# Performance work log

Measured on AMD Instinct MI355X. Metric: run time of the kernel, lower is better.

The kernel has to match this reference:

```python
import jax, jax.numpy as jnp
import numpy as np

H = 450    # hidden_size (JTNN default)
LAT = 56   # latent_size (tree_vec dim)
V = 780    # vocab size
T = 1024   # n_trees
L = 24     # nodes per tree (path topology)


def _tree_meta(Ln):
    # forward edge i: (i, i+1) eid=i ; reverse edge i: (i+1, i) eid=(Ln-1)+i
    n_f = Ln - 1
    eids, preds, srcs, dsts, labels = [], [], [], [], []
    for i in range(n_f):  # forward DFS steps
        eids.append(i); srcs.append(i); dsts.append(i + 1)
        preds.append(i - 1 if i > 0 else -1); labels.append(0)
    for k in range(n_f):  # backtrack DFS steps (reverse edges, deepest first)
        i = n_f - 1 - k
        eids.append(n_f + i); srcs.append(i + 1); dsts.append(i)
        preds.append(n_f + i + 1 if i < n_f - 1 else -1); labels.append(1)
    # incoming edges of the dst node v (for the node 'pull' h = sum of m)
    in1 = [d - 1 if d > 0 else -1 for d in dsts]
    in2 = [n_f + d if d < n_f else -1 for d in dsts]
    meta = [np.asarray(a, np.int32) for a in (eids, preds, srcs, dsts, in1, in2)]
    return meta, np.asarray(labels, np.float32)


def setup_inputs():
    key = jax.random.key(0)
    ks = jax.random.split(key, 12)
    s = 0.05
    return {
        "wid": jax.random.randint(ks[0], (T, L), 0, V, dtype=jnp.int32),
        "tree_vec": jax.random.normal(ks[1], (T, LAT), jnp.float32),
        "emb": jax.random.normal(ks[2], (V, H)) * s,
        "W_w": jax.random.normal(ks[3], (H + LAT, H)) * s, "W_b": jnp.zeros((H,)),
        "U_w": jax.random.normal(ks[4], (2 * H + LAT, H)) * s, "U_b": jnp.zeros((H,)),
        "Wo_w": jax.random.normal(ks[5], (H, V)) * s, "Wo_b": jnp.zeros((V,)),
        "Us_w": jax.random.normal(ks[6], (H, 1)) * s, "Us_b": jnp.zeros((1,)),
        "Wz_w": jax.random.normal(ks[7], (2 * H, H)) * s, "Wz_b": jnp.zeros((H,)),
        "Wr_w": jax.random.normal(ks[8], (H, H)) * s,
        "Ur_w": jax.random.normal(ks[9], (H, H)) * s, "Ur_b": jnp.zeros((H,)),
        "Wh_w": jax.random.normal(ks[10], (2 * H, H)) * s, "Wh_b": jnp.zeros((H,)),
    }


def reference(wid, tree_vec, emb, W_w, W_b, U_w, U_b, Wo_w, Wo_b, Us_w, Us_b,
              Wz_w, Wz_b, Wr_w, Ur_w, Ur_b, Wh_w, Wh_b):
    Tn, Ln = wid.shape
    n_f = Ln - 1
    nE = 2 * n_f
    meta, labels = _tree_meta(Ln)
    xs = tuple(jnp.asarray(a) for a in meta)
    x = emb[wid]                                  # [T, L, H] node features
    m0 = jnp.zeros((Tn, nE, H), x.dtype)
    rm0 = jnp.zeros((Tn, nE, H), x.dtype)

    def step(carry, sx_):
        m, rm = carry
        eid, pred, src, dst, i1, i2 = sx_
        gp = jnp.maximum(pred, 0)
        s = jnp.where(pred >= 0, m[:, gp], 0.0)        # line-graph pull: sum of m
        arm = jnp.where(pred >= 0, rm[:, gp], 0.0)     # accum_rm
        sxn = x[:, src]                                # src_x
        dxn = x[:, dst]                                # dst_x
        z = jax.nn.sigmoid(jnp.concatenate([sxn, s], 1) @ Wz_w + Wz_b)
        mt = jnp.tanh(jnp.concatenate([sxn, arm], 1) @ Wh_w + Wh_b)
        m_new = (1.0 - z) * s + z * mt
        r = jax.nn.sigmoid(dxn @ Wr_w + m_new @ Ur_w + Ur_b)
        m = m.at[:, eid].set(m_new)
        rm = rm.at[:, eid].set(r * m_new)
        # node pull on v: h_v = sum of m over incoming edges (post edge update)
        h_v = (jnp.where(i1 >= 0, m[:, jnp.maximum(i1, 0)], 0.0)
               + jnp.where(i2 >= 0, m[:, jnp.maximum(i2, 0)], 0.0))
        return (m, rm), (h_v, dxn)

    (_, _), (hs, xvs) = jax.lax.scan(step, (m0, rm0), xs)  # [nE, T, H] each

    tv_steps = jnp.broadcast_to(tree_vec, (nE, Tn, LAT))
    p_in = jnp.concatenate([
        jnp.concatenate([x[:, 0], jnp.zeros((Tn, H), x.dtype), tree_vec], 1),
        jnp.concatenate([xvs, hs, tv_steps], -1).reshape(-1, 2 * H + LAT),
    ], 0)
    q_in = jnp.concatenate([
        jnp.concatenate([jnp.zeros((Tn, H), x.dtype), tree_vec], 1),
        jnp.concatenate([hs[:n_f], tv_steps[:n_f]], -1).reshape(-1, H + LAT),
    ], 0)
    p_targets = jnp.concatenate([jnp.repeat(jnp.asarray(1.0 - labels), Tn),
                                 jnp.zeros((Tn,), jnp.float32)])
    q_targets = wid.T.reshape(-1)

    q_logits = jax.nn.relu(q_in @ W_w + W_b) @ Wo_w + Wo_b
    p_logit = (jax.nn.relu(p_in @ U_w + U_b) @ Us_w + Us_b)[:, 0]
    p_loss = jnp.sum(p_targets * jax.nn.softplus(-p_logit)
                     + (1.0 - p_targets) * jax.nn.softplus(p_logit)) / Tn
    logp = jax.nn.log_softmax(q_logits, -1)
    q_loss = -jnp.sum(jnp.take_along_axis(logp, q_targets[:, None], 1)) / Tn
    p_acc = jnp.mean(((p_logit > 0).astype(jnp.int32) == p_targets.astype(jnp.int32)).astype(jnp.float32))
    q_acc = jnp.mean((jnp.argmax(q_logits, 1) == q_targets).astype(jnp.float32))
    return (q_loss, p_loss, q_acc, p_acc)
```

## Files before the change

kernel.cpp:

```cpp
#include <hip/hip_runtime.h>
#include <hip/hip_bf16.h>
#include <math.h>

#define H 450
#define HP 464
#define KP 480
#define LAT 56
#define V 780
#define LW 24
#define NE 46
#define NF 23
#define SLOT (1024*HP)
#define SROWS 2048
#define QROWS (24*1024)
#define PROWS (47*1024)
#define PTGT  (23*1024)
#define QBLK 6144
#define XBSZ ((size_t)QROWS * HP)
#define BTROWS 5312

typedef __hip_bfloat16 bf16;
typedef __attribute__((ext_vector_type(8))) short short8;
typedef __attribute__((ext_vector_type(4))) float f32x4;

#define MFMA16(a,b,c) __builtin_amdgcn_mfma_f32_16x16x32_bf16(a,b,c,0,0,0)

__device__ __forceinline__ float sigm_f(float x) { return 1.f / (1.f + __expf(-x)); }
__device__ __forceinline__ float tanh_f(float x) { return 2.f / (1.f + __expf(-2.f * x)) - 1.f; }
__device__ __forceinline__ float toF(bf16 x) { return __bfloat162float(x); }
__device__ __forceinline__ void stV(float* p, float v) { *p = v; }
__device__ __forceinline__ void stV(bf16* p, float v) { *p = __float2bfloat16(v); }
__device__ __forceinline__ short8 ld8(const bf16* p) { return *reinterpret_cast<const short8*>(p); }

__device__ __forceinline__ void gl_lds(const bf16* g, bf16* l) {
    __builtin_amdgcn_global_load_lds(
        (const __attribute__((address_space(1))) void*)g,
        (__attribute__((address_space(3))) void*)l, 16, 0, 0);
}

__device__ __forceinline__ void xcd_decode128(int b, int C, int& row0, int& col0) {
    int rres = b & 7;
    int colt = (b >> 3) % C;
    int g    = b / (8 * C);
    row0 = (rres + 8 * g) * 128;
    col0 = colt * 128;
}

__global__ __launch_bounds__(256)
void prep_w(const float* __restrict__ Wz, const float* __restrict__ Wh,
            const float* __restrict__ Wr, const float* __restrict__ Uw,
            const float* __restrict__ Ww, const float* __restrict__ Wo,
            const float* __restrict__ Ur, bf16* __restrict__ BT) {
    int idx = blockIdx.x * 256 + threadIdx.x;
    if (idx >= BTROWS * KP) return;
    int r = idx / KP, k = idx - r * KP;
    const float* src; int n; int N = H; int ld = H;
    if (r < 1856) {
        if (r < 450)       { src = Wz; n = r; }
        else if (r < 900)  { src = Wh; n = r - 450; }
        else if (r < 1350) { src = Wr; n = r - 900; }
        else               { src = Uw; n = r - 1350; }
    } else if (r < 2368) { src = Wz + 450 * 450; n = r - 1856; }
    else if (r < 2880)   { src = Wh + 450 * 450; n = r - 2368; }
    else if (r < 3392)   { src = Ur;             n = r - 2880; }
    else if (r < 3904)   { src = Uw + 450 * 450; n = r - 3392; }
    else if (r < 4416)   { src = Ww;             n = r - 3904; }
    else                 { src = Wo; n = r - 4416; N = V; ld = V; }
    float v = (n < N && k < H) ? src[(size_t)k * ld + n] : 0.f;
    BT[idx] = __float2bfloat16(v);
}

__global__ __launch_bounds__(256)
void pack_misc(const float* __restrict__ zb, const float* __restrict__ hb,
               const float* __restrict__ rb, float* __restrict__ bias4,
               float* __restrict__ out) {
    int i = blockIdx.x * 256 + threadIdx.x;
    if (i < 4) out[i] = 0.f;
    if (i >= 1856) return;
    float v = 0.f;
    if (i < 450)       v = zb[i];
    else if (i < 900)  v = hb[i - 450];
    else if (i < 1350) v = rb[i - 900];
    bias4[i] = v;
}

__global__ __launch_bounds__(256)
void gather_x(const float* __restrict__ emb, const int* __restrict__ wid,
              bf16* __restrict__ x_all) {
    int e = blockIdx.x * 256 + threadIdx.x;
    if (e >= 24 * 1024 * 225) return;
    int row = e / 225, h2 = e - row * 225;
    int t = row >> 10, n = row & 1023;
    int v = wid[n * LW + t];
    float2 x = ((const float2*)(emb + (size_t)v * H))[h2];
    bf16* dst = x_all + (size_t)row * HP + 2 * h2;
    dst[0] = __float2bfloat16(x.x);
    dst[1] = __float2bfloat16(x.y);
}

template<typename TC>
__global__ __launch_bounds__(256)
void gemm128(const bf16* __restrict__ A, int lda,
             const bf16* __restrict__ Bt, int N, int cblk,
             TC* __restrict__ C, int ldc,
             const float* __restrict__ bias,
             const float* __restrict__ addrow, int addld, int relu) {
    __shared__ bf16 As[128 * 32];
    __shared__ bf16 Bs[128 * 32];
    int tid = threadIdx.x;
    int lane = tid & 63, wave = tid >> 6;
    int wx = wave & 1, wy = wave >> 1;
    int lrow = lane & 15, quad = lane >> 4;
    int perm = ((quad + (lrow >> 1)) & 3) * 8;
    int row0, col0;
    xcd_decode128(blockIdx.x, cblk, row0, col0);
    f32x4 acc[4][4] = {};
    for (int k0i = 0; k0i < 15; k0i++) {
        int k0 = k0i * 32;
#pragma unroll
        for (int r = 0; r < 2; r++) {
            int tt = r * 256 + tid;
            int row = tt >> 2, cl = tt & 3;
            int cg = (cl - (row >> 1)) & 3;
            gl_lds(A  + (size_t)(row0 + row) * lda + k0 + cg * 8, As + tt * 8);
            gl_lds(Bt + (size_t)(col0 + row) * KP  + k0 + cg * 8, Bs + tt * 8);
        }
        __syncthreads();
        short8 a[4], b[4];
#pragma unroll
        for (int f = 0; f < 4; f++)
            a[f] = ld8(As + (wy * 64 + f * 16 + lrow) * 32 + perm);
#pragma unroll
        for (int f = 0; f < 4; f++)
            b[f] = ld8(Bs + (wx * 64 + f * 16 + lrow) * 32 + perm);
#pragma unroll
        for (int fi = 0; fi < 4; fi++)
#pragma unroll
            for (int fj = 0; fj < 4; fj++)
                acc[fi][fj] = MFMA16(a[fi], b[fj], acc[fi][fj]);
        __syncthreads();
    }
#pragma unroll
    for (int fi = 0; fi < 4; fi++)
#pragma unroll
        for (int e = 0; e < 4; e++) {
            int r = row0 + wy * 64 + fi * 16 + quad * 4 + e;
#pragma unroll
            for (int fj = 0; fj < 4; fj++) {
                int c = col0 + wx * 64 + fj * 16 + lrow;
                if (c >= N) continue;
                float v = acc[fi][fj][e];
                if (bias) v += bias[c];
                if (addrow) v += addrow[(size_t)(r & 1023) * addld + c];
                if (relu) v = fmaxf(v, 0.f);
                stV(&C[(size_t)r * ldc + c], v);
            }
        }
}

__global__ __launch_bounds__(256)
void gemm128_pre(const bf16* __restrict__ A,
                 const bf16* __restrict__ Bt,
                 bf16* __restrict__ X0,
                 const float* __restrict__ bias4) {
    __shared__ bf16 As[128 * 32];
    __shared__ bf16 Bs[128 * 32];
    int tid = threadIdx.x;
    int lane = tid & 63, wave = tid >> 6;
    int wx = wave & 1, wy = wave >> 1;
    int lrow = lane & 15, quad = lane >> 4;
    int perm = ((quad + (lrow >> 1)) & 3) * 8;
    int row0, col0;
    xcd_decode128(blockIdx.x, 15, row0, col0);
    f32x4 acc[4][4] = {};
    for (int k0i = 0; k0i < 15; k0i++) {
        int k0 = k0i * 32;
#pragma unroll
        for (int r = 0; r < 2; r++) {
            int tt = r * 256 + tid;
            int row = tt >> 2, cl = tt & 3;
            int cg = (cl - (row >> 1)) & 3;
            gl_lds(A  + (size_t)(row0 + row) * HP + k0 + cg * 8, As + tt * 8);
            gl_lds(Bt + (size_t)(col0 + row) * KP + k0 + cg * 8, Bs + tt * 8);
        }
        __syncthreads();
        short8 a[4], b[4];
#pragma unroll
        for (int f = 0; f < 4; f++)
            a[f] = ld8(As + (wy * 64 + f * 16 + lrow) * 32 + perm);
#pragma unroll
        for (int f = 0; f < 4; f++)
            b[f] = ld8(Bs + (wx * 64 + f * 16 + lrow) * 32 + perm);
#pragma unroll
        for (int fi = 0; fi < 4; fi++)
#pragma unroll
            for (int fj = 0; fj < 4; fj++)
                acc[fi][fj] = MFMA16(a[fi], b[fj], acc[fi][fj]);
        __syncthreads();
    }
#pragma unroll
    for (int fi = 0; fi < 4; fi++)
#pragma unroll
        for (int e = 0; e < 4; e++) {
            int r = row0 + wy * 64 + fi * 16 + quad * 4 + e;
#pragma unroll
            for (int fj = 0; fj < 4; fj++) {
                int c = col0 + wx * 64 + fj * 16 + lrow;
                if (c >= 1800) continue;
                int mm = c / 450;
                int cc = c - mm * 450;
                float v = acc[fi][fj][e] + bias4[c];
                X0[(size_t)mm * XBSZ + (size_t)r * HP + cc] = __float2bfloat16(v);
            }
        }
}

__global__ __launch_bounds__(256)
void p_gemm128(const bf16* __restrict__ hs, const bf16* __restrict__ UbT,
               const bf16* __restrict__ XUa, const float* __restrict__ Ptv,
               const float* __restrict__ Us, float* __restrict__ pl) {
    __shared__ bf16 As[128 * 32];
    __shared__ bf16 Bs[128 * 32];
    int tid = threadIdx.x;
    int lane = tid & 63, wave = tid >> 6;
    int wx = wave & 1, wy = wave >> 1;
    int lrow = lane & 15, quad = lane >> 4;
    int perm = ((quad + (lrow >> 1)) & 3) * 8;
    int row0, col0;
    xcd_decode128(blockIdx.x, 4, row0, col0);
    f32x4 acc[4][4] = {};
    for (int k0i = 0; k0i < 15; k0i++) {
        int k0 = k0i * 32;
#pragma unroll
        for (int r = 0; r < 2; r++) {
            int tt = r * 256 + tid;
            int row = tt >> 2, cl = tt & 3;
            int cg = (cl - (row >> 1)) & 3;
            gl_lds(hs  + (size_t)(row0 + row) * HP + k0 + cg * 8, As + tt * 8);
            gl_lds(UbT + (size_t)(col0 + row) * KP + k0 + cg * 8, Bs + tt * 8);
        }
        __syncthreads();
        short8 a[4], b[4];
#pragma unroll
        for (int f = 0; f < 4; f++)
            a[f] = ld8(As + (wy * 64 + f * 16 + lrow) * 32 + perm);
#pragma unroll
        for (int f = 0; f < 4; f++)
            b[f] = ld8(Bs + (wx * 64 + f * 16 + lrow) * 32 + perm);
#pragma unroll
        for (int fi = 0; fi < 4; fi++)
#pragma unroll
            for (int fj = 0; fj < 4; fj++)
                acc[fi][fj] = MFMA16(a[fi], b[fj], acc[fi][fj]);
        __syncthreads();
    }
#pragma unroll
    for (int fi = 0; fi < 4; fi++)
#pragma unroll
        for (int e = 0; e < 4; e++) {
            int r = row0 + wy * 64 + fi * 16 + quad * 4 + e;
            int t = r >> 10, n = r & 1023;
            int dst = (t < 23) ? (t + 1) : (45 - t);
            float part = 0.f;
#pragma unroll
            for (int fj = 0; fj < 4; fj++) {
                int c = col0 + wx * 64 + fj * 16 + lrow;
                if (c < H) {
                    float h = fmaxf(acc[fi][fj][e] + toF(XUa[((size_t)dst * 1024 + n) * HP + c])
                                    + Ptv[(size_t)n * H + c], 0.f);
                    part += h * Us[c];
                }
            }
#pragma unroll
            for (int off = 1; off < 16; off <<= 1)
                part += __shfl_xor(part, off);
            if (lrow == 0) atomicAdd(&pl[1024 + r], part);
        }
}

__global__ __launch_bounds__(256)
void tv_gemm(const float* __restrict__ tv, const float* __restrict__ Wlat,
             const float* __restrict__ bias, float* __restrict__ out) {
    int n = blockIdx.y;
    int c = blockIdx.x * 256 + threadIdx.x;
    __shared__ float tvs[LAT];
    if (threadIdx.x < LAT) tvs[threadIdx.x] = tv[n * LAT + threadIdx.x];
    __syncthreads();
    if (c < H) {
        float a = bias[c];
#pragma unroll 8
        for (int k = 0; k < LAT; k++) a += tvs[k] * Wlat[(size_t)k * H + c];
        out[(size_t)n * H + c] = a;
    }
}

__global__ __launch_bounds__(1024)
void scan_full(bf16* __restrict__ hs,
               const bf16* __restrict__ WzbT, const bf16* __restrict__ WhbT,
               const bf16* __restrict__ UrT,
               const bf16* __restrict__ Xz, const bf16* __restrict__ Xh,
               const bf16* __restrict__ Xr) {
    __shared__ bf16 mnl[2][16][488];
    __shared__ bf16 rml[16][488];
    __shared__ bf16 xzs[16][464];
    __shared__ bf16 xhs[16][464];
    __shared__ bf16 xrs[16][464];
    int tid = threadIdx.x;
    int lane = tid & 63, w = tid >> 6;
    int lrow = lane & 15, quad = lane >> 4;
    int row0 = blockIdx.x * 16;
    bool fwd = row0 < 1024;
    int nb = row0 & 1023;
    int f0 = w, f1 = w + 16;
    bool hasf1 = (f1 < 29);
    int crow = tid / 58, cj = tid - crow * 58;
    bool cok = tid < 928;
    float sreg[2][4];
#pragma unroll
    for (int i = 0; i < 2; i++)
#pragma unroll
        for (int e = 0; e < 4; e++) sreg[i][e] = 0.f;
    for (int i = tid; i < 2 * 16 * 488; i += 1024) ((bf16*)mnl)[i] = __float2bfloat16(0.f);
    for (int i = tid; i < 16 * 488; i += 1024) ((bf16*)rml)[i] = __float2bfloat16(0.f);
    __syncthreads();

    for (int u = 0; u < 23; u++) {
        int cur = u & 1, prev = cur ^ 1;
        int src = fwd ? u : 23 - u;
        int dst = fwd ? (u + 1) : (22 - u);
        float4 vz, vh, vr;
        if (cok) {
            vz = *reinterpret_cast<const float4*>(Xz + ((size_t)src * 1024 + nb + crow) * HP + cj * 8);
            vh = *reinterpret_cast<const float4*>(Xh + ((size_t)src * 1024 + nb + crow) * HP + cj * 8);
            if (u < 22)
                vr = *reinterpret_cast<const float4*>(Xr + ((size_t)dst * 1024 + nb + crow) * HP + cj * 8);
        }
        f32x4 az[2], ah[2];
#pragma unroll
        for (int i = 0; i < 2; i++) {
            az[i] = (f32x4){0.f, 0.f, 0.f, 0.f};
            ah[i] = (f32x4){0.f, 0.f, 0.f, 0.f};
        }
        if (u > 0) {
            for (int k = 0; k < 15; k++) {
                short8 sA = *reinterpret_cast<const short8*>(&mnl[prev][lrow][k * 32 + quad * 8]);
                short8 rA = *reinterpret_cast<const short8*>(&rml[lrow][k * 32 + quad * 8]);
                {
                    short8 zB = ld8(WzbT + (size_t)(f0 * 16 + lrow) * KP + k * 32 + quad * 8);
                    short8 hB = ld8(WhbT + (size_t)(f0 * 16 + lrow) * KP + k * 32 + quad * 8);
                    az[0] = MFMA16(sA, zB, az[0]);
                    ah[0] = MFMA16(rA, hB, ah[0]);
                }
                if (hasf1) {
                    short8 zB = ld8(WzbT + (size_t)(f1 * 16 + lrow) * KP + k * 32 + quad * 8);
                    short8 hB = ld8(WhbT + (size_t)(f1 * 16 + lrow) * KP + k * 32 + quad * 8);
                    az[1] = MFMA16(sA, zB, az[1]);
                    ah[1] = MFMA16(rA, hB, ah[1]);
                }
            }
        }
        if (cok) {
            *reinterpret_cast<float4*>(&xzs[crow][cj * 8]) = vz;
            *reinterpret_cast<float4*>(&xhs[crow][cj * 8]) = vh;
            if (u < 22)
                *reinterpret_cast<float4*>(&xrs[crow][cj * 8]) = vr;
        }
        __syncthreads();

        int hsl = fwd ? u : 23 + u;
        bf16* hso = hs + (size_t)hsl * SLOT;
#pragma unroll
        for (int i = 0; i < 2; i++) {
            int f = (i == 0) ? f0 : f1;
            if (i == 1 && !hasf1) break;
            int c = f * 16 + lrow;
            if (c < H) {
#pragma unroll
                for (int e = 0; e < 4; e++) {
                    int rl = quad * 4 + e;
                    int n = (row0 + rl) & 1023;
                    float zp = az[i][e] + toF(xzs[rl][c]);
                    float hp = ah[i][e] + toF(xhs[rl][c]);
                    float z = sigm_f(zp), mt = tanh_f(hp);
                    float mn = (1.f - z) * sreg[i][e] + z * mt;
                    sreg[i][e] = mn;
                    bf16 mb = __float2bfloat16(mn);
                    mnl[cur][rl][c] = mb;
                    hso[(size_t)n * HP + c] = mb;
                }
            }
        }
        __syncthreads();

        if (u < 22) {
            f32x4 ar[2];
#pragma unroll
            for (int i = 0; i < 2; i++) ar[i] = (f32x4){0.f, 0.f, 0.f, 0.f};
            for (int k = 0; k < 15; k++) {
                short8 a = *reinterpret_cast<const short8*>(&mnl[cur][lrow][k * 32 + quad * 8]);
                ar[0] = MFMA16(a, ld8(UrT + (size_t)(f0 * 16 + lrow) * KP + k * 32 + quad * 8), ar[0]);
                if (hasf1)
                    ar[1] = MFMA16(a, ld8(UrT + (size_t)(f1 * 16 + lrow) * KP + k * 32 + quad * 8), ar[1]);
            }
#pragma unroll
            for (int i = 0; i < 2; i++) {
                int f = (i == 0) ? f0 : f1;
                if (i == 1 && !hasf1) break;
                int c = f * 16 + lrow;
                if (c < H) {
#pragma unroll
                    for (int e = 0; e < 4; e++) {
                        int rl = quad * 4 + e;
                        float rp = ar[i][e] + toF(xrs[rl][c]);
                        rml[rl][c] = __float2bfloat16(sigm_f(rp) * toF(mnl[cur][rl][c]));
                    }
                }
            }
            __syncthreads();
        }
    }
}

__global__ __launch_bounds__(256)
void hv_fixup(bf16* __restrict__ hs) {
    int idx = blockIdx.x * 256 + threadIdx.x;
    if (idx >= 22 * SLOT) return;
    int tl = idx / SLOT;
    int rem = idx - tl * SLOT;
    size_t a = (size_t)(23 + tl) * SLOT + rem;
    size_t b = (size_t)(21 - tl) * SLOT + rem;
    hs[a] = __float2bfloat16(toF(hs[a]) + toF(hs[b]));
}

__global__ __launch_bounds__(256)
void q_root(const float* __restrict__ Qtv, bf16* __restrict__ qh) {
    int idx = blockIdx.x * 256 + threadIdx.x;
    if (idx >= 1024 * H) return;
    int n = idx / H, c = idx - n * H;
    qh[(size_t)n * HP + c] = __float2bfloat16(fmaxf(Qtv[idx], 0.f));
}

__global__ __launch_bounds__(256)
void q_reduce(const float* __restrict__ ql, const int* __restrict__ wid,
              float* __restrict__ qred) {
    int wave = threadIdx.x >> 6, lane = threadIdx.x & 63;
    int r = blockIdx.x * 4 + wave;
    int t = r >> 10, n = r & 1023;
    int tgt = wid[n * LW + t];
    const float4* row4 = (const float4*)(ql + (size_t)r * V);
    float m = -3.4e38f, s = 0.f; int mi = 0x7fffffff;
#pragma unroll
    for (int k = 0; k < 4; k++) {
        int c4 = lane + 64 * k;
        if (c4 < 195) {
            float4 v4 = row4[c4];
            float vv[4] = {v4.x, v4.y, v4.z, v4.w};
#pragma unroll
            for (int e = 0; e < 4; e++) {
                float v = vv[e];
                if (v > m) { s = s * __expf(m - v) + 1.f; m = v; mi = c4 * 4 + e; }
                else s += __expf(v - m);
            }
        }
    }
#pragma unroll
    for (int off = 1; off < 64; off <<= 1) {
        float m2 = __shfl_xor(m, off);
        float s2 = __shfl_xor(s, off);
        int   i2 = __shfl_xor(mi, off);
        if (m2 > m || (m2 == m && i2 < mi)) {
            s = s2 + s * __expf(m - m2);
            m = m2; mi = i2;
        } else {
            s = s + s2 * __expf(m2 - m);
        }
    }
    __shared__ float lred[4][2];
    if (lane == 0) {
        float lse = m + logf(s);
        lred[wave][0] = lse - ql[(size_t)r * V + tgt];
        lred[wave][1] = (mi == tgt) ? 1.f : 0.f;
    }
    __syncthreads();
    if (threadIdx.x == 0) {
        qred[blockIdx.x * 2]     = lred[0][0] + lred[1][0] + lred[2][0] + lred[3][0];
        qred[blockIdx.x * 2 + 1] = lred[0][1] + lred[1][1] + lred[2][1] + lred[3][1];
    }
}

__global__ __launch_bounds__(256)
void q_final(const float* __restrict__ qred, float* __restrict__ out) {
    int tid = threadIdx.x;
    float L = 0.f, A = 0.f;
    for (int i = tid; i < QBLK; i += 256) { L += qred[2 * i]; A += qred[2 * i + 1]; }
    __shared__ float s1[256], s2[256];
    s1[tid] = L; s2[tid] = A;
    __syncthreads();
    for (int k = 128; k > 0; k >>= 1) {
        if (tid < k) { s1[tid] += s1[tid + k]; s2[tid] += s2[tid + k]; }
        __syncthreads();
    }
    if (tid == 0) {
        out[0] = s1[0] * (1.f / 1024.f);
        out[2] = s2[0] * (1.f / 24576.f);
    }
}

__global__ __launch_bounds__(256)
void p_init(float* __restrict__ pl, const float* __restrict__ Us_b) {
    int idx = blockIdx.x * 256 + threadIdx.x;
    if (idx < PROWS) pl[idx] = Us_b[0];
}

__global__ __launch_bounds__(256)
void p_root(const bf16* __restrict__ XUa, const float* __restrict__ Ptv,
            const float* __restrict__ Us, float* __restrict__ pl) {
    int n = blockIdx.x;
    int tid = threadIdx.x;
    const bf16* xa = XUa + (size_t)n * HP;
    const float* pt = Ptv + (size_t)n * H;
    float s = 0.f;
    for (int c = tid; c < H; c += 256)
        s += fmaxf(toF(xa[c]) + pt[c], 0.f) * Us[c];
    __shared__ float red[256];
    red[tid] = s;
    __syncthreads();
    for (int k = 128; k > 0; k >>= 1) {
        if (tid < k) red[tid] += red[tid + k];
        __syncthreads();
    }
    if (tid == 0) atomicAdd(&pl[n], red[0]);
}

__global__ __launch_bounds__(256)
void p_final(const float* __restrict__ pl, float* __restrict__ out) {
    int r = blockIdx.x * 256 + threadIdx.x;
    int tid = threadIdx.x;
    float loss = 0.f, acc = 0.f;
    if (r < PROWS) {
        float l = pl[r];
        int tgt = (r < PTGT) ? 1 : 0;
        float x = tgt ? -l : l;
        loss = fmaxf(x, 0.f) + log1pf(expf(-fabsf(x)));
        int pred = (l > 0.f) ? 1 : 0;
        acc = (pred == tgt) ? 1.f : 0.f;
    }
    __shared__ float s1[256], s2[256];
    s1[tid] = loss; s2[tid] = acc;
    __syncthreads();
    for (int k = 128; k > 0; k >>= 1) {
        if (tid < k) { s1[tid] += s1[tid + k]; s2[tid] += s2[tid + k]; }
        __syncthreads();
    }
    if (tid == 0) {
        atomicAdd(&out[1], s1[0] * (1.f / 1024.f));
        atomicAdd(&out[3], s2[0] * (1.f / 48128.f));
    }
}

extern "C" void kernel_launch(void* const* d_in, const int* in_sizes, int n_in,
                              void* d_out, int out_size, void* d_ws, size_t ws_size,
                              hipStream_t stream) {
    const int*   wid  = (const int*)  d_in[0];
    const float* tv   = (const float*)d_in[1];
    const float* emb  = (const float*)d_in[2];
    const float* W_w  = (const float*)d_in[3];
    const float* W_b  = (const float*)d_in[4];
    const float* U_w  = (const float*)d_in[5];
    const float* U_b  = (const float*)d_in[6];
    const float* Wo_w = (const float*)d_in[7];
    const float* Wo_b = (const float*)d_in[8];
    const float* Us_w = (const float*)d_in[9];
    const float* Us_b = (const float*)d_in[10];
    const float* Wz_w = (const float*)d_in[11];
    const float* Wz_b = (const float*)d_in[12];
    const float* Wr_w = (const float*)d_in[13];
    const float* Ur_w = (const float*)d_in[14];
    const float* Ur_b = (const float*)d_in[15];
    const float* Wh_w = (const float*)d_in[16];
    const float* Wh_b = (const float*)d_in[17];
    float* out = (float*)d_out;

    char* base = (char*)d_ws;
    const size_t XBb = XBSZ * 2;
    bf16*  Xz   = (bf16*)(base);
    bf16*  Xh   = (bf16*)(base + XBb);
    bf16*  Xr   = (bf16*)(base + 2 * XBb);
    bf16*  XUa  = (bf16*)(base + 3 * XBb);
    bf16*  hs   = (bf16*)(base + 4 * XBb);
    bf16*  x_all = hs;
    char*  p1   = base + 4 * XBb + (size_t)NE * SLOT * 2;
    float* Qtv  = (float*)p1;               p1 += (size_t)1024 * H * 4;
    float* Ptv  = (float*)p1;               p1 += (size_t)1024 * H * 4;
    float* pl   = (float*)p1;               p1 += (size_t)PROWS * 4;
    float* qred = (float*)p1;               p1 += (size_t)QBLK * 2 * 4;
    float* bias4 = (float*)p1;              p1 += (size_t)1856 * 4;
    bf16*  BT   = (bf16*)p1;
    bf16* BT4   = BT;
    bf16* WzbT  = BT + (size_t)1856 * KP;
    bf16* WhbT  = WzbT + (size_t)512 * KP;
    bf16* UrT   = WhbT + (size_t)512 * KP;
    bf16* UbT   = UrT  + (size_t)512 * KP;
    bf16* WtopT = UbT  + (size_t)512 * KP;
    bf16* WoT   = WtopT + (size_t)512 * KP;
    bf16*  qh = (bf16*)base;
    float* ql = (float*)(base + (size_t)QROWS * HP * 2);

    pack_misc<<<8, 256, 0, stream>>>(Wz_b, Wh_b, Ur_b, bias4, out);
    prep_w<<<(BTROWS * KP + 255) / 256, 256, 0, stream>>>(Wz_w, Wh_w, Wr_w, U_w,
                                                          W_w, Wo_w, Ur_w, BT);

    gather_x<<<(24 * 1024 * 225 + 255) / 256, 256, 0, stream>>>(emb, wid, x_all);
    gemm128_pre<<<(QROWS / 128) * 15, 256, 0, stream>>>(x_all, BT4, Xz, bias4);

    tv_gemm<<<dim3(2, 1024), 256, 0, stream>>>(tv, W_w + 450*450, W_b, Qtv);
    tv_gemm<<<dim3(2, 1024), 256, 0, stream>>>(tv, U_w + 900*450, U_b, Ptv);

    scan_full<<<SROWS / 16, 1024, 0, stream>>>(hs, WzbT, WhbT, UrT, Xz, Xh, Xr);
    hv_fixup<<<(22 * SLOT + 255) / 256, 256, 0, stream>>>(hs);

    p_init<<<(PROWS + 255) / 256, 256, 0, stream>>>(pl, Us_b);
    p_root<<<1024, 256, 0, stream>>>(XUa, Ptv, Us_w, pl);
    p_gemm128<<<(PROWS - 1024) / 128 * 4, 256, 0, stream>>>(hs, UbT, XUa, Ptv, Us_w, pl);
    p_final<<<PROWS / 256, 256, 0, stream>>>(pl, out);

    q_root<<<(1024 * H + 255) / 256, 256, 0, stream>>>(Qtv, qh);
    gemm128<bf16><<<(NF * 1024 / 128) * 4, 256, 0, stream>>>(hs, HP, WtopT, H, 4,
                                                             qh + (size_t)1024 * HP, HP,
                                                             (const float*)nullptr, Qtv, H, 1);
    gemm128<float><<<(QROWS / 128) * 7, 256, 0, stream>>>(qh, HP, WoT, V, 7, ql, V,
                                                          Wo_b, (const float*)nullptr, H, 0);
    q_reduce<<<QBLK, 256, 0, stream>>>(ql, wid, qred);
    q_final<<<1, 256, 0, stream>>>(qred, out);

    (void)in_sizes; (void)n_in; (void)out_size; (void)ws_size;
}
```

Measured before the change: 1.222 ms.

## Compact pre-activation stride, drop scan LDS staging, store logits in bf16

Pre-activation buffers Xz/Xh/Xr/XUa now use a row stride of H instead of the padded HP. The scan kernel reads them directly from global memory in its epilogue instead of staging them through shared memory with an extra barrier. The vocab logits GEMM now writes bf16 instead of fp32, which halves the traffic that q_reduce reads. The p_init kernel is replaced by a memset, with the bias folded into p_final. Risks are unaligned, uncoalesced gathers inside the latency-bound scan and lower logit precision affecting the loss and argmax.

```diff
diff --git a/kernel.cpp b/kernel.cpp
--- a/kernel.cpp
+++ b/kernel.cpp
@@ -16,11 +16,12 @@
 #define PROWS (47*1024)
 #define PTGT  (23*1024)
 #define QBLK 6144
-#define XBSZ ((size_t)QROWS * HP)
+#define XBSZ ((size_t)QROWS * H)
 #define BTROWS 5312
 
 typedef __hip_bfloat16 bf16;
 typedef __attribute__((ext_vector_type(8))) short short8;
+typedef __attribute__((ext_vector_type(4))) short short4v;
 typedef __attribute__((ext_vector_type(4))) float f32x4;
 
 #define MFMA16(a,b,c) __builtin_amdgcn_mfma_f32_16x16x32_bf16(a,b,c,0,0,0)
@@ -28,6 +29,10 @@
 __device__ __forceinline__ float sigm_f(float x) { return 1.f / (1.f + __expf(-x)); }
 __device__ __forceinline__ float tanh_f(float x) { return 2.f / (1.f + __expf(-2.f * x)) - 1.f; }
 __device__ __forceinline__ float toF(bf16 x) { return __bfloat162float(x); }
+__device__ __forceinline__ float bf2f(short s) {
+    unsigned u = ((unsigned)(unsigned short)s) << 16;
+    return __uint_as_float(u);
+}
 __device__ __forceinline__ void stV(float* p, float v) { *p = v; }
 __device__ __forceinline__ void stV(bf16* p, float v) { *p = __float2bfloat16(v); }
 __device__ __forceinline__ short8 ld8(const bf16* p) { return *reinterpret_cast<const short8*>(p); }
@@ -210,7 +215,7 @@
                 int mm = c / 450;
                 int cc = c - mm * 450;
                 float v = acc[fi][fj][e] + bias4[c];
-                X0[(size_t)mm * XBSZ + (size_t)r * HP + cc] = __float2bfloat16(v);
+                X0[(size_t)mm * XBSZ + (size_t)r * H + cc] = __float2bfloat16(v);
             }
         }
 }
@@ -266,7 +271,7 @@
             for (int fj = 0; fj < 4; fj++) {
                 int c = col0 + wx * 64 + fj * 16 + lrow;
                 if (c < H) {
-                    float h = fmaxf(acc[fi][fj][e] + toF(XUa[((size_t)dst * 1024 + n) * HP + c])
+                    float h = fmaxf(acc[fi][fj][e] + toF(XUa[((size_t)dst * 1024 + n) * H + c])
                                     + Ptv[(size_t)n * H + c], 0.f);
                     part += h * Us[c];
                 }
@@ -302,19 +307,13 @@
                const bf16* __restrict__ Xr) {
     __shared__ bf16 mnl[2][16][488];
     __shared__ bf16 rml[16][488];
-    __shared__ bf16 xzs[16][464];
-    __shared__ bf16 xhs[16][464];
-    __shared__ bf16 xrs[16][464];
     int tid = threadIdx.x;
     int lane = tid & 63, w = tid >> 6;
     int lrow = lane & 15, quad = lane >> 4;
     int row0 = blockIdx.x * 16;
     bool fwd = row0 < 1024;
-    int nb = row0 & 1023;
     int f0 = w, f1 = w + 16;
     bool hasf1 = (f1 < 29);
-    int crow = tid / 58, cj = tid - crow * 58;
-    bool cok = tid < 928;
     float sreg[2][4];
 #pragma unroll
     for (int i = 0; i < 2; i++)
@@ -326,15 +325,6 @@
 
     for (int u = 0; u < 23; u++) {
         int cur = u & 1, prev = cur ^ 1;
-        int src = fwd ? u : 23 - u;
-        int dst = fwd ? (u + 1) : (22 - u);
-        float4 vz, vh, vr;
-        if (cok) {
-            vz = *reinterpret_cast<const float4*>(Xz + ((size_t)src * 1024 + nb + crow) * HP + cj * 8);
-            vh = *reinterpret_cast<const float4*>(Xh + ((size_t)src * 1024 + nb + crow) * HP + cj * 8);
-            if (u < 22)
-                vr = *reinterpret_cast<const float4*>(Xr + ((size_t)dst * 1024 + nb + crow) * HP + cj * 8);
-        }
         f32x4 az[2], ah[2];
 #pragma unroll
         for (int i = 0; i < 2; i++) {
@@ -359,16 +349,8 @@
                 }
             }
         }
-        if (cok) {
-            *reinterpret_cast<float4*>(&xzs[crow][cj * 8]) = vz;
-            *reinterpret_cast<float4*>(&xhs[crow][cj * 8]) = vh;
-            if (u < 22)
-                *reinterpret_cast<float4*>(&xrs[crow][cj * 8]) = vr;
-        }
-        __syncthreads();
-
-        int hsl = fwd ? u : 23 + u;
-        bf16* hso = hs + (size_t)hsl * SLOT;
+        int src = fwd ? u : 23 - u;
+        bf16* hso = hs + (size_t)(fwd ? u : 23 + u) * SLOT;
 #pragma unroll
         for (int i = 0; i < 2; i++) {
             int f = (i == 0) ? f0 : f1;
@@ -379,8 +361,8 @@
                 for (int e = 0; e < 4; e++) {
                     int rl = quad * 4 + e;
                     int n = (row0 + rl) & 1023;
-                    float zp = az[i][e] + toF(xzs[rl][c]);
-                    float hp = ah[i][e] + toF(xhs[rl][c]);
+                    float zp = az[i][e] + toF(Xz[((size_t)src * 1024 + n) * H + c]);
+                    float hp = ah[i][e] + toF(Xh[((size_t)src * 1024 + n) * H + c]);
                     float z = sigm_f(zp), mt = tanh_f(hp);
                     float mn = (1.f - z) * sreg[i][e] + z * mt;
                     sreg[i][e] = mn;
@@ -402,6 +384,7 @@
                 if (hasf1)
                     ar[1] = MFMA16(a, ld8(UrT + (size_t)(f1 * 16 + lrow) * KP + k * 32 + quad * 8), ar[1]);
             }
+            int dst = fwd ? (u + 1) : (22 - u);
 #pragma unroll
             for (int i = 0; i < 2; i++) {
                 int f = (i == 0) ? f0 : f1;
@@ -411,7 +394,8 @@
 #pragma unroll
                     for (int e = 0; e < 4; e++) {
                         int rl = quad * 4 + e;
-                        float rp = ar[i][e] + toF(xrs[rl][c]);
+                        int n = (row0 + rl) & 1023;
+                        float rp = ar[i][e] + toF(Xr[((size_t)dst * 1024 + n) * H + c]);
                         rml[rl][c] = __float2bfloat16(sigm_f(rp) * toF(mnl[cur][rl][c]));
                     }
                 }
@@ -441,23 +425,22 @@
 }
 
 __global__ __launch_bounds__(256)
-void q_reduce(const float* __restrict__ ql, const int* __restrict__ wid,
+void q_reduce(const bf16* __restrict__ ql, const int* __restrict__ wid,
               float* __restrict__ qred) {
     int wave = threadIdx.x >> 6, lane = threadIdx.x & 63;
     int r = blockIdx.x * 4 + wave;
     int t = r >> 10, n = r & 1023;
     int tgt = wid[n * LW + t];
-    const float4* row4 = (const float4*)(ql + (size_t)r * V);
+    const short4v* row4 = (const short4v*)(ql + (size_t)r * V);
     float m = -3.4e38f, s = 0.f; int mi = 0x7fffffff;
 #pragma unroll
     for (int k = 0; k < 4; k++) {
         int c4 = lane + 64 * k;
         if (c4 < 195) {
-            float4 v4 = row4[c4];
-            float vv[4] = {v4.x, v4.y, v4.z, v4.w};
+            short4v v4 = row4[c4];
 #pragma unroll
             for (int e = 0; e < 4; e++) {
-                float v = vv[e];
+                float v = bf2f(v4[e]);
                 if (v > m) { s = s * __expf(m - v) + 1.f; m = v; mi = c4 * 4 + e; }
                 else s += __expf(v - m);
             }
@@ -478,7 +461,7 @@
     __shared__ float lred[4][2];
     if (lane == 0) {
         float lse = m + logf(s);
-        lred[wave][0] = lse - ql[(size_t)r * V + tgt];
+        lred[wave][0] = lse - toF(ql[(size_t)r * V + tgt]);
         lred[wave][1] = (mi == tgt) ? 1.f : 0.f;
     }
     __syncthreads();
@@ -507,17 +490,11 @@
 }
 
 __global__ __launch_bounds__(256)
-void p_init(float* __restrict__ pl, const float* __restrict__ Us_b) {
-    int idx = blockIdx.x * 256 + threadIdx.x;
-    if (idx < PROWS) pl[idx] = Us_b[0];
-}
-
-__global__ __launch_bounds__(256)
 void p_root(const bf16* __restrict__ XUa, const float* __restrict__ Ptv,
             const float* __restrict__ Us, float* __restrict__ pl) {
     int n = blockIdx.x;
     int tid = threadIdx.x;
-    const bf16* xa = XUa + (size_t)n * HP;
+    const bf16* xa = XUa + (size_t)n * H;
     const float* pt = Ptv + (size_t)n * H;
     float s = 0.f;
     for (int c = tid; c < H; c += 256)
@@ -529,16 +506,18 @@
         if (tid < k) red[tid] += red[tid + k];
         __syncthreads();
     }
-    if (tid == 0) atomicAdd(&pl[n], red[0]);
-}
-
-__global__ __launch_bounds__(256)
-void p_final(const float* __restrict__ pl, float* __restrict__ out) {
+    if (tid == 0) pl[n] = red[0];
+}
+
+__global__ __launch_bounds__(256)
+void p_final(const float* __restrict__ pl, const float* __restrict__ Us_b,
+             float* __restrict__ out) {
     int r = blockIdx.x * 256 + threadIdx.x;
     int tid = threadIdx.x;
+    float ub = Us_b[0];
     float loss = 0.f, acc = 0.f;
     if (r < PROWS) {
-        float l = pl[r];
+        float l = pl[r] + ub;
         int tgt = (r < PTGT) ? 1 : 0;
         float x = tgt ? -l : l;
         loss = fmaxf(x, 0.f) + log1pf(expf(-fabsf(x)));
@@ -604,9 +583,10 @@
     bf16* WtopT = UbT  + (size_t)512 * KP;
     bf16* WoT   = WtopT + (size_t)512 * KP;
     bf16*  qh = (bf16*)base;
-    float* ql = (float*)(base + (size_t)QROWS * HP * 2);
+    bf16*  ql = (bf16*)(base + (size_t)QROWS * HP * 2);
 
     pack_misc<<<8, 256, 0, stream>>>(Wz_b, Wh_b, Ur_b, bias4, out);
+    hipMemsetAsync(pl, 0, (size_t)PROWS * 4, stream);
     prep_w<<<(BTROWS * KP + 255) / 256, 256, 0, stream>>>(Wz_w, Wh_w, Wr_w, U_w,
                                                           W_w, Wo_w, Ur_w, BT);
 
@@ -619,17 +599,16 @@
     scan_full<<<SROWS / 16, 1024, 0, stream>>>(hs, WzbT, WhbT, UrT, Xz, Xh, Xr);
     hv_fixup<<<(22 * SLOT + 255) / 256, 256, 0, stream>>>(hs);
 
-    p_init<<<(PROWS + 255) / 256, 256, 0, stream>>>(pl, Us_b);
     p_root<<<1024, 256, 0, stream>>>(XUa, Ptv, Us_w, pl);
     p_gemm128<<<(PROWS - 1024) / 128 * 4, 256, 0, stream>>>(hs, UbT, XUa, Ptv, Us_w, pl);
-    p_final<<<PROWS / 256, 256, 0, stream>>>(pl, out);
+    p_final<<<PROWS / 256, 256, 0, stream>>>(pl, Us_b, out);
 
     q_root<<<(1024 * H + 255) / 256, 256, 0, stream>>>(Qtv, qh);
     gemm128<bf16><<<(NF * 1024 / 128) * 4, 256, 0, stream>>>(hs, HP, WtopT, H, 4,
                                                              qh + (size_t)1024 * HP, HP,
                                                              (const float*)nullptr, Qtv, H, 1);
-    gemm128<float><<<(QROWS / 128) * 7, 256, 0, stream>>>(qh, HP, WoT, V, 7, ql, V,
-                                                          Wo_b, (const float*)nullptr, H, 0);
+    gemm128<bf16><<<(QROWS / 128) * 7, 256, 0, stream>>>(qh, HP, WoT, V, 7, ql, V,
+                                                         Wo_b, (const float*)nullptr, H, 0);
     q_reduce<<<QBLK, 256, 0, stream>>>(ql, wid, qred);
     q_final<<<1, 256, 0, stream>>>(qred, out);
 
```

Result: faster. 1.007 ms (-17.6%).
